# Kernel optimization log

Measured on AMD Instinct MI355X. Metric: run time of the kernel, lower is better.

The kernel has to match this reference:

```python
import jax, jax.numpy as jnp
import numpy as np
import math

RES = 2048
EGG_FACTOR = 0.25
BUMP_STRENGTH = 1.0
SPEC_POWER = 32.0
AMBIENT = 0.1
_L = np.array([0.5, 0.7, 1.0], dtype=np.float32)
LIGHT = _L / np.sqrt((_L * _L).sum())
VIEW = np.array([0.0, 0.0, 1.0], dtype=np.float32)
F0 = np.float32(((1.5 - 1.0) / (1.5 + 1.0)) ** 2)  # Schlick F0 from IOR=1.5 -> 0.04


def _pixel_grid():
    # matches torch.meshgrid(x, y, indexing='xy') ray generation buffers
    x = np.arange(RES, dtype=np.float32)
    y = np.arange(RES, dtype=np.float32)
    px, py = np.meshgrid(x, y, indexing='xy')
    scale = 0.85
    nx = (px / RES - 0.5) * 2.0 / scale
    ny = (0.5 - py / RES) * 2.0 / scale
    return jnp.asarray(nx), jnp.asarray(ny)


def sample_bilinear(tex, u, v):
    # BilinearSampler with UV wrap; tex: (H, W, C), u/v: (...,)
    h, w = tex.shape[0], tex.shape[1]
    u = u % 1.0
    v = v % 1.0
    x = u * w - 0.5
    y = v * h - 0.5
    x0 = jnp.floor(x).astype(jnp.int32) % w
    y0 = jnp.floor(y).astype(jnp.int32) % h
    x1 = (x0 + 1) % w
    y1 = (y0 + 1) % h
    fx = (x - jnp.floor(x))[..., None]
    fy = (y - jnp.floor(y))[..., None]
    v00 = tex[y0, x0]
    v01 = tex[y0, x1]
    v10 = tex[y1, x0]
    v11 = tex[y1, x1]
    return (v00 * (1 - fx) * (1 - fy) + v01 * fx * (1 - fy)
            + v10 * (1 - fx) * fy + v11 * fx * fy)


def _tbn(n):
    # Gram-Schmidt tangent frame from surface normal field, (..., 3)
    up = jnp.zeros_like(n).at[..., 1].set(1.0)
    right = jnp.zeros_like(n).at[..., 0].set(1.0)
    dot_up = n[..., 1]
    ref = jnp.where((jnp.abs(dot_up) > 0.99)[..., None], right, up)
    t = ref - jnp.sum(ref * n, axis=-1, keepdims=True) * n
    t = t / jnp.clip(jnp.linalg.norm(t, axis=-1, keepdims=True), 1e-6)
    b = jnp.cross(n, t)
    return t, b


def reference(texture, normal_map):
    nx, ny = _pixel_grid()
    # 1-2. ray-sphere intersection
    r_sq = nx * nx + ny * ny
    inside = r_sq <= 1.0
    z = jnp.sqrt(jnp.clip(1.0 - r_sq, 0.0))
    # 3. egg deformation
    egg_mod = 1.0 - EGG_FACTOR * ny
    safe = jnp.abs(egg_mod) > 0.01
    x_egg = jnp.where(safe, nx / egg_mod, nx)
    z_egg = jnp.where(safe, z / egg_mod, z)
    # 4. spherical UV
    phi = jnp.arccos(jnp.clip(ny, -1.0, 1.0))
    theta = jnp.arctan2(z_egg, x_egg)
    u = (theta / (2.0 * math.pi) + 0.5) % 1.0
    v = phi / math.pi
    # 5. texture / normal-map sampling
    albedo = sample_bilinear(texture, u, v)
    tex_n = sample_bilinear(normal_map, u, v) * 2.0 - 1.0  # [0,1] -> [-1,1]
    # 6. analytical egg normal + TBN frame
    sn = jnp.stack([nx * egg_mod, ny, z * egg_mod], axis=-1)
    base_n = sn / jnp.clip(jnp.linalg.norm(sn, axis=-1, keepdims=True), 1e-6)
    tangent, bitangent = _tbn(base_n)
    # 7. normal perturbation
    world_n = (tex_n[..., 0:1] * tangent + tex_n[..., 1:2] * bitangent
               + tex_n[..., 2:3] * base_n)
    nrm = base_n * (1.0 - BUMP_STRENGTH) + world_n * BUMP_STRENGTH
    nrm = nrm / jnp.clip(jnp.linalg.norm(nrm, axis=-1, keepdims=True), 1e-6)
    # 8. Blinn-Phong + Schlick Fresnel lighting
    light = jnp.asarray(LIGHT)
    view = jnp.asarray(VIEW)
    half = light + view
    half = half / jnp.linalg.norm(half)
    ndotl = jnp.clip(jnp.sum(nrm * light, axis=-1), 0.0)
    ndoth = jnp.clip(jnp.sum(nrm * half, axis=-1), 0.0)
    spec = ndoth ** SPEC_POWER
    ndotv = jnp.clip(jnp.sum(nrm * view, axis=-1), 0.0)
    fres = F0 + (1.0 - F0) * (1.0 - ndotv) ** 5
    color = albedo * (AMBIENT + ndotl)[..., None] + (spec * fres)[..., None]
    color = jnp.clip(color, 0.0, 1.0)
    return jnp.where(inside[..., None], color, 0.0)


def setup_inputs():
    key = jax.random.key(0)
    k1, k2 = jax.random.split(key)
    texture = jax.random.uniform(k1, (1024, 1024, 3), dtype=jnp.float32)
    normal_map = jax.random.uniform(k2, (1024, 1024, 3), dtype=jnp.float32)
    return {"texture": texture, "normal_map": normal_map}
```

## Files before the change

### kernel.cpp

```cpp
#include <hip/hip_runtime.h>
#include <math.h>

#define RESN 2048
#define TEXW 1024

__device__ __forceinline__ float fatan2_pos(float y, float x) {
    float ax = fabsf(x);
    float mn = fminf(ax, y);
    float mx = fmaxf(ax, y);
    float r0 = __builtin_amdgcn_rcpf(mx);
    r0 = r0 * __builtin_fmaf(-mx, r0, 2.0f);
    float a = mn * r0;
    bool red = a > 0.41421356f;
    float t = (a - 1.0f) * __builtin_amdgcn_rcpf(a + 1.0f);
    float w = red ? t : a;
    float s = w * w;
    float p = __builtin_fmaf(s, 8.05374449538e-2f, -1.38776856032e-1f);
    p = __builtin_fmaf(s, p, 1.99777106478e-1f);
    p = __builtin_fmaf(s, p, -3.33329491539e-1f);
    float r = __builtin_fmaf(w * s, p, w);
    r = red ? r + 0.78539816339f : r;
    r = (y > ax) ? 1.57079632679f - r : r;
    r = (x < 0.0f) ? 3.14159265359f - r : r;
    return r;
}

struct __align__(4) F3 { float x, y, z; };

__global__ __launch_bounds__(256) void egg_render(
    const float* __restrict__ tex,
    const float* __restrict__ nmap,
    float* __restrict__ out)
{
    int t = blockIdx.x * 256 + threadIdx.x;
    int j = t >> 10;
    int tr = t & 1023;
    int iA = ((tr >> 6) << 7) + (tr & 63);
    int iB = iA + 64;
    float* oA = out + ((size_t)j * RESN + iA) * 3u;
    float* oB = oA + 192u;

    const float invres = 1.0f / (float)RESN;
    float ny = __fmul_rn(__fsub_rn(0.5f, __fmul_rn((float)j, invres)), 2.0f) / 0.85f;
    float nysq = __fmul_rn(ny, ny);

    if (!(nysq <= 1.0f)) {
        oA[0] = 0.f; oA[1] = 0.f; oA[2] = 0.f;
        oB[0] = 0.f; oB[1] = 0.f; oB[2] = 0.f;
        return;
    }

    float egg = 1.0f - 0.25f * ny;
    float sphi = sqrtf(fmaxf(__builtin_fmaf(-ny, ny, 1.0f), 0.0f));
    float phi = fatan2_pos(sphi, ny);
    float v = phi * 0.3183098861837907f;
    float yy = v * (float)TEXW - 0.5f;
    float yf = floorf(yy);
    float fy = yy - yf;
    float gy = 1.0f - fy;
    int y0 = (int)yf & (TEXW - 1);
    int y1 = (y0 + 1) & (TEXW - 1);
    int rb0 = y0 * TEXW;
    int rb1 = y1 * TEXW;

    float nxA = __fmul_rn(__fsub_rn(__fmul_rn((float)iA, invres), 0.5f), 2.0f) / 0.85f;
    float rsqA = __fadd_rn(__fmul_rn(nxA, nxA), nysq);
    bool inA = (rsqA <= 1.0f);
    float zA = sqrtf(fmaxf(__fsub_rn(1.0f, rsqA), 0.0f));
    float thetaA = fatan2_pos(zA, nxA);
    float uA = thetaA * 0.15915494309189535f + 0.5f;
    float xxA = uA * (float)TEXW - 0.5f;
    float xfA = floorf(xxA);
    float fxA = xxA - xfA;
    float gxA = 1.0f - fxA;
    int x0A = (int)xfA & (TEXW - 1);
    int x1A = (x0A + 1) & (TEXW - 1);
    float w00A = gxA * gy, w01A = fxA * gy, w10A = gxA * fy, w11A = fxA * fy;
    int o00A = (rb0 + x0A) * 3, o01A = (rb0 + x1A) * 3;
    int o10A = (rb1 + x0A) * 3, o11A = (rb1 + x1A) * 3;

    float nxB = __fmul_rn(__fsub_rn(__fmul_rn((float)iB, invres), 0.5f), 2.0f) / 0.85f;
    float rsqB = __fadd_rn(__fmul_rn(nxB, nxB), nysq);
    bool inB = (rsqB <= 1.0f);
    float zB = sqrtf(fmaxf(__fsub_rn(1.0f, rsqB), 0.0f));
    float thetaB = fatan2_pos(zB, nxB);
    float uB = thetaB * 0.15915494309189535f + 0.5f;
    float xxB = uB * (float)TEXW - 0.5f;
    float xfB = floorf(xxB);
    float fxB = xxB - xfB;
    float gxB = 1.0f - fxB;
    int x0B = (int)xfB & (TEXW - 1);
    int x1B = (x0B + 1) & (TEXW - 1);
    float w00B = gxB * gy, w01B = fxB * gy, w10B = gxB * fy, w11B = fxB * fy;
    int o00B = (rb0 + x0B) * 3, o01B = (rb0 + x1B) * 3;
    int o10B = (rb1 + x0B) * 3, o11B = (rb1 + x1B) * 3;

    if (!(__any((int)inA) || __any((int)inB))) {
        oA[0] = 0.f; oA[1] = 0.f; oA[2] = 0.f;
        oB[0] = 0.f; oB[1] = 0.f; oB[2] = 0.f;
        return;
    }

    F3 aA00 = *(const F3*)(tex + o00A);
    F3 aA01 = *(const F3*)(tex + o01A);
    F3 aA10 = *(const F3*)(tex + o10A);
    F3 aA11 = *(const F3*)(tex + o11A);
    F3 nA00 = *(const F3*)(nmap + o00A);
    F3 nA01 = *(const F3*)(nmap + o01A);
    F3 nA10 = *(const F3*)(nmap + o10A);
    F3 nA11 = *(const F3*)(nmap + o11A);
    F3 aB00 = *(const F3*)(tex + o00B);
    F3 aB01 = *(const F3*)(tex + o01B);
    F3 aB10 = *(const F3*)(tex + o10B);
    F3 aB11 = *(const F3*)(tex + o11B);
    F3 nB00 = *(const F3*)(nmap + o00B);
    F3 nB01 = *(const F3*)(nmap + o01B);
    F3 nB10 = *(const F3*)(nmap + o10B);
    F3 nB11 = *(const F3*)(nmap + o11B);

    float Lx = 0.5f, Ly = 0.7f, Lz = 1.0f;
    float ll = sqrtf(Lx * Lx + Ly * Ly + Lz * Lz);
    Lx /= ll; Ly /= ll; Lz /= ll;
    float Hx = Lx, Hy = Ly, Hz = Lz + 1.0f;
    float hl = sqrtf(Hx * Hx + Hy * Hy + Hz * Hz);
    Hx /= hl; Hy /= hl; Hz /= hl;

    {
        float ar = aA00.x*w00A + aA01.x*w01A + aA10.x*w10A + aA11.x*w11A;
        float ag = aA00.y*w00A + aA01.y*w01A + aA10.y*w10A + aA11.y*w11A;
        float ab = aA00.z*w00A + aA01.z*w01A + aA10.z*w10A + aA11.z*w11A;
        float tnx = (nA00.x*w00A + nA01.x*w01A + nA10.x*w10A + nA11.x*w11A) * 2.0f - 1.0f;
        float tny = (nA00.y*w00A + nA01.y*w01A + nA10.y*w10A + nA11.y*w11A) * 2.0f - 1.0f;
        float tnz = (nA00.z*w00A + nA01.z*w01A + nA10.z*w10A + nA11.z*w11A) * 2.0f - 1.0f;

        float snx = nxA * egg, sny = ny, snz = zA * egg;
        float sl2 = snx*snx + sny*sny + snz*snz;
        float isl = __builtin_amdgcn_rsqf(sl2);
        float bnx = snx * isl, bny = sny * isl, bnz = snz * isl;

        bool use_right = fabsf(bny) > 0.99f;
        float d = use_right ? bnx : bny;
        float m = use_right ? bny : bnx;
        float q2 = m * m + bnz * bnz;
        float iq = __builtin_amdgcn_rsqf(q2);
        float q  = q2 * iq;
        float e  = -(d * iq);
        float tzv = bnz * e;
        float tx = use_right ? q : (bnx * e);
        float ty = use_right ? (bny * e) : q;
        float bnxiq = bnx * iq, bnyiq = bny * iq, bnziq = bnz * iq;
        float bx = use_right ? 0.0f   : -bnziq;
        float by = use_right ? bnziq  : 0.0f;
        float bz = use_right ? -bnyiq : bnxiq;

        float wx = tnx * tx + tny * bx + tnz * bnx;
        float wy = tnx * ty + tny * by + tnz * bny;
        float wz = tnx * tzv + tny * bz + tnz * bnz;
        float wl2 = wx*wx + wy*wy + wz*wz;
        float iwl = __builtin_amdgcn_rsqf(fmaxf(wl2, 1e-12f));
        wx *= iwl; wy *= iwl; wz *= iwl;

        float ndotl = fmaxf(wx * Lx + wy * Ly + wz * Lz, 0.0f);
        float ndoth = fmaxf(wx * Hx + wy * Hy + wz * Hz, 0.0f);
        float s2 = ndoth * ndoth, s4 = s2 * s2, s8 = s4 * s4, s16 = s8 * s8;
        float spec = s16 * s16;
        float ndotv = fmaxf(wz, 0.0f);
        float t1 = 1.0f - ndotv;
        float t2 = t1 * t1, t4 = t2 * t2;
        float fres = 0.04f + 0.96f * (t4 * t1);
        float ka = 0.1f + ndotl;
        float add = spec * fres;

        oA[0] = inA ? fminf(fmaxf(__builtin_fmaf(ar, ka, add), 0.0f), 1.0f) : 0.0f;
        oA[1] = inA ? fminf(fmaxf(__builtin_fmaf(ag, ka, add), 0.0f), 1.0f) : 0.0f;
        oA[2] = inA ? fminf(fmaxf(__builtin_fmaf(ab, ka, add), 0.0f), 1.0f) : 0.0f;
    }

    {
        float ar = aB00.x*w00B + aB01.x*w01B + aB10.x*w10B + aB11.x*w11B;
        float ag = aB00.y*w00B + aB01.y*w01B + aB10.y*w10B + aB11.y*w11B;
        float ab = aB00.z*w00B + aB01.z*w01B + aB10.z*w10B + aB11.z*w11B;
        float tnx = (nB00.x*w00B + nB01.x*w01B + nB10.x*w10B + nB11.x*w11B) * 2.0f - 1.0f;
        float tny = (nB00.y*w00B + nB01.y*w01B + nB10.y*w10B + nB11.y*w11B) * 2.0f - 1.0f;
        float tnz = (nB00.z*w00B + nB01.z*w01B + nB10.z*w10B + nB11.z*w11B) * 2.0f - 1.0f;

        float snx = nxB * egg, sny = ny, snz = zB * egg;
        float sl2 = snx*snx + sny*sny + snz*snz;
        float isl = __builtin_amdgcn_rsqf(sl2);
        float bnx = snx * isl, bny = sny * isl, bnz = snz * isl;

        bool use_right = fabsf(bny) > 0.99f;
        float d = use_right ? bnx : bny;
        float m = use_right ? bny : bnx;
        float q2 = m * m + bnz * bnz;
        float iq = __builtin_amdgcn_rsqf(q2);
        float q  = q2 * iq;
        float e  = -(d * iq);
        float tzv = bnz * e;
        float tx = use_right ? q : (bnx * e);
        float ty = use_right ? (bny * e) : q;
        float bnxiq = bnx * iq, bnyiq = bny * iq, bnziq = bnz * iq;
        float bx = use_right ? 0.0f   : -bnziq;
        float by = use_right ? bnziq  : 0.0f;
        float bz = use_right ? -bnyiq : bnxiq;

        float wx = tnx * tx + tny * bx + tnz * bnx;
        float wy = tnx * ty + tny * by + tnz * bny;
        float wz = tnx * tzv + tny * bz + tnz * bnz;
        float wl2 = wx*wx + wy*wy + wz*wz;
        float iwl = __builtin_amdgcn_rsqf(fmaxf(wl2, 1e-12f));
        wx *= iwl; wy *= iwl; wz *= iwl;

        float ndotl = fmaxf(wx * Lx + wy * Ly + wz * Lz, 0.0f);
        float ndoth = fmaxf(wx * Hx + wy * Hy + wz * Hz, 0.0f);
        float s2 = ndoth * ndoth, s4 = s2 * s2, s8 = s4 * s4, s16 = s8 * s8;
        float spec = s16 * s16;
        float ndotv = fmaxf(wz, 0.0f);
        float t1 = 1.0f - ndotv;
        float t2 = t1 * t1, t4 = t2 * t2;
        float fres = 0.04f + 0.96f * (t4 * t1);
        float ka = 0.1f + ndotl;
        float add = spec * fres;

        oB[0] = inB ? fminf(fmaxf(__builtin_fmaf(ar, ka, add), 0.0f), 1.0f) : 0.0f;
        oB[1] = inB ? fminf(fmaxf(__builtin_fmaf(ag, ka, add), 0.0f), 1.0f) : 0.0f;
        oB[2] = inB ? fminf(fmaxf(__builtin_fmaf(ab, ka, add), 0.0f), 1.0f) : 0.0f;
    }
}

extern "C" void kernel_launch(void* const* d_in, const int* in_sizes, int n_in,
                              void* d_out, int out_size, void* d_ws, size_t ws_size,
                              hipStream_t stream) {
    const float* tex  = (const float*)d_in[0];
    const float* nmap = (const float*)d_in[1];
    float* out = (float*)d_out;
    int total_threads = RESN * RESN / 2;
    dim3 grid(total_threads / 256), block(256);
    hipLaunchKernelGGL(egg_render, grid, block, 0, stream, tex, nmap, out);
}
```

Baseline: 26.32 us.

## Repack texture and normal map into half-precision interleaved records in workspace

Adds a pre-pass kernel that gathers only the half of the texture columns the visible hemisphere can sample, converts albedo and normal to fp16 and interleaves them into one 16-byte record per texel. The render kernel then does four 16-byte loads per sample instead of eight scattered 12-byte loads. This reduces gather traffic and the number of load instructions, at the cost of an extra kernel launch, a full pass over the inputs in every call, and fp16 rounding of the texture data. The wave-level early-out for fully outside waves is dropped, and a fallback path is kept for when workspace is too small.

```diff
diff --git a/kernel.cpp b/kernel.cpp
--- a/kernel.cpp
+++ b/kernel.cpp
@@ -1,8 +1,12 @@
 #include <hip/hip_runtime.h>
+#include <hip/hip_fp16.h>
 #include <math.h>
 
 #define RESN 2048
 #define TEXW 1024
+#define PW 514
+#define PH 1025
+#define PREC (PH * PW)
 
 __device__ __forceinline__ float fatan2_pos(float y, float x) {
     float ax = fabsf(x);
@@ -26,8 +30,176 @@
 }
 
 struct __align__(4) F3 { float x, y, z; };
-
-__global__ __launch_bounds__(256) void egg_render(
+union HU { uint4 v; __half h[8]; };
+
+__global__ __launch_bounds__(256) void repack(const float* __restrict__ tex,
+                                              const float* __restrict__ nmap,
+                                              uint4* __restrict__ rec) {
+    int idx = blockIdx.x * 256 + threadIdx.x;
+    if (idx >= PREC) return;
+    int y  = idx / PW;
+    int rx = idx - y * PW;
+    int sx = (rx + 511) & (TEXW - 1);
+    int sy = y & (TEXW - 1);
+    int s = (sy * TEXW + sx) * 3;
+    HU u;
+    u.h[0] = __float2half(tex[s + 0]);
+    u.h[1] = __float2half(tex[s + 1]);
+    u.h[2] = __float2half(tex[s + 2]);
+    u.h[3] = __float2half(nmap[s + 0]);
+    u.h[4] = __float2half(nmap[s + 1]);
+    u.h[5] = __float2half(nmap[s + 2]);
+    u.h[6] = __float2half(0.0f);
+    u.h[7] = __float2half(0.0f);
+    rec[idx] = u.v;
+}
+
+#define BLEND6(c00, c01, c10, c11, w00, w01, w10, w11, ar, ag, ab, tnx, tny, tnz)          \
+    ar  = __half2float(c00.h[0])*w00 + __half2float(c01.h[0])*w01                          \
+        + __half2float(c10.h[0])*w10 + __half2float(c11.h[0])*w11;                         \
+    ag  = __half2float(c00.h[1])*w00 + __half2float(c01.h[1])*w01                          \
+        + __half2float(c10.h[1])*w10 + __half2float(c11.h[1])*w11;                         \
+    ab  = __half2float(c00.h[2])*w00 + __half2float(c01.h[2])*w01                          \
+        + __half2float(c10.h[2])*w10 + __half2float(c11.h[2])*w11;                         \
+    tnx = (__half2float(c00.h[3])*w00 + __half2float(c01.h[3])*w01                         \
+        +  __half2float(c10.h[3])*w10 + __half2float(c11.h[3])*w11) * 2.0f - 1.0f;         \
+    tny = (__half2float(c00.h[4])*w00 + __half2float(c01.h[4])*w01                         \
+        +  __half2float(c10.h[4])*w10 + __half2float(c11.h[4])*w11) * 2.0f - 1.0f;         \
+    tnz = (__half2float(c00.h[5])*w00 + __half2float(c01.h[5])*w01                         \
+        +  __half2float(c10.h[5])*w10 + __half2float(c11.h[5])*w11) * 2.0f - 1.0f;
+
+#define SHADE(nx, z, tnx, tny, tnz, ar, ag, ab, inx, o)                                    \
+    {                                                                                      \
+        float snx = nx * egg, sny = ny, snz = z * egg;                                     \
+        float sl2 = snx*snx + sny*sny + snz*snz;                                           \
+        float isl = __builtin_amdgcn_rsqf(sl2);                                            \
+        float bnx = snx * isl, bny = sny * isl, bnz = snz * isl;                           \
+        bool use_right = fabsf(bny) > 0.99f;                                               \
+        float d = use_right ? bnx : bny;                                                   \
+        float m = use_right ? bny : bnx;                                                   \
+        float q2 = m * m + bnz * bnz;                                                      \
+        float iq = __builtin_amdgcn_rsqf(q2);                                              \
+        float q  = q2 * iq;                                                                \
+        float e  = -(d * iq);                                                              \
+        float tzv = bnz * e;                                                               \
+        float tx = use_right ? q : (bnx * e);                                              \
+        float ty = use_right ? (bny * e) : q;                                              \
+        float bx = use_right ? 0.0f        : -(bnz * iq);                                  \
+        float by = use_right ? (bnz * iq)  : 0.0f;                                         \
+        float bz = use_right ? -(bny * iq) : (bnx * iq);                                   \
+        float wx = tnx * tx + tny * bx + tnz * bnx;                                        \
+        float wy = tnx * ty + tny * by + tnz * bny;                                        \
+        float wz = tnx * tzv + tny * bz + tnz * bnz;                                       \
+        float wl2 = wx*wx + wy*wy + wz*wz;                                                 \
+        float iwl = __builtin_amdgcn_rsqf(fmaxf(wl2, 1e-12f));                             \
+        wx *= iwl; wy *= iwl; wz *= iwl;                                                   \
+        float ndotl = fmaxf(wx * Lx + wy * Ly + wz * Lz, 0.0f);                            \
+        float ndoth = fmaxf(wx * Hx + wy * Hy + wz * Hz, 0.0f);                            \
+        float s2 = ndoth * ndoth, s4 = s2 * s2, s8 = s4 * s4, s16 = s8 * s8;               \
+        float spec = s16 * s16;                                                            \
+        float ndotv = fmaxf(wz, 0.0f);                                                     \
+        float t1 = 1.0f - ndotv;                                                           \
+        float t2v = t1 * t1, t4v = t2v * t2v;                                              \
+        float fres = 0.04f + 0.96f * (t4v * t1);                                           \
+        float ka = 0.1f + ndotl;                                                           \
+        float add = spec * fres;                                                           \
+        o[0] = inx ? fminf(fmaxf(__builtin_fmaf(ar, ka, add), 0.0f), 1.0f) : 0.0f;         \
+        o[1] = inx ? fminf(fmaxf(__builtin_fmaf(ag, ka, add), 0.0f), 1.0f) : 0.0f;         \
+        o[2] = inx ? fminf(fmaxf(__builtin_fmaf(ab, ka, add), 0.0f), 1.0f) : 0.0f;         \
+    }
+
+__global__ __launch_bounds__(256) void egg_render_packed(
+    const uint4* __restrict__ rec,
+    float* __restrict__ out)
+{
+    int t = blockIdx.x * 256 + threadIdx.x;
+    int j = t >> 10;
+    int tr = t & 1023;
+    int iA = ((tr >> 6) << 7) + (tr & 63);
+    int iB = iA + 64;
+    float* oA = out + ((size_t)j * RESN + iA) * 3u;
+    float* oB = oA + 192u;
+
+    const float invres = 1.0f / (float)RESN;
+    float ny = __fmul_rn(__fsub_rn(0.5f, __fmul_rn((float)j, invres)), 2.0f) / 0.85f;
+    float nysq = __fmul_rn(ny, ny);
+
+    if (!(nysq <= 1.0f)) {
+        oA[0] = 0.f; oA[1] = 0.f; oA[2] = 0.f;
+        oB[0] = 0.f; oB[1] = 0.f; oB[2] = 0.f;
+        return;
+    }
+
+    float egg = 1.0f - 0.25f * ny;
+    float sphi = sqrtf(fmaxf(__builtin_fmaf(-ny, ny, 1.0f), 0.0f));
+    float phi = fatan2_pos(sphi, ny);
+    float v = phi * 0.3183098861837907f;
+    float yy = v * (float)TEXW - 0.5f;
+    float yf = floorf(yy);
+    float fy = yy - yf;
+    float gy = 1.0f - fy;
+    int y0 = (int)yf & (TEXW - 1);
+    int rb0 = y0 * PW;
+    int rb1 = rb0 + PW;
+
+    float nxA = __fmul_rn(__fsub_rn(__fmul_rn((float)iA, invres), 0.5f), 2.0f) / 0.85f;
+    float rsqA = __fadd_rn(__fmul_rn(nxA, nxA), nysq);
+    bool inA = (rsqA <= 1.0f);
+    float zA = sqrtf(fmaxf(__fsub_rn(1.0f, rsqA), 0.0f));
+    float thetaA = fatan2_pos(zA, nxA);
+    float uA = thetaA * 0.15915494309189535f + 0.5f;
+    float xxA = uA * (float)TEXW - 0.5f;
+    float xfA = floorf(xxA);
+    float fxA = xxA - xfA;
+    float gxA = 1.0f - fxA;
+    int rxA = min(max((int)xfA - 511, 0), 512);
+    float w00A = gxA * gy, w01A = fxA * gy, w10A = gxA * fy, w11A = fxA * fy;
+
+    HU cA00, cA01, cA10, cA11;
+    cA00.v = rec[rb0 + rxA];
+    cA01.v = rec[rb0 + rxA + 1];
+    cA10.v = rec[rb1 + rxA];
+    cA11.v = rec[rb1 + rxA + 1];
+
+    float nxB = __fmul_rn(__fsub_rn(__fmul_rn((float)iB, invres), 0.5f), 2.0f) / 0.85f;
+    float rsqB = __fadd_rn(__fmul_rn(nxB, nxB), nysq);
+    bool inB = (rsqB <= 1.0f);
+    float zB = sqrtf(fmaxf(__fsub_rn(1.0f, rsqB), 0.0f));
+    float thetaB = fatan2_pos(zB, nxB);
+    float uB = thetaB * 0.15915494309189535f + 0.5f;
+    float xxB = uB * (float)TEXW - 0.5f;
+    float xfB = floorf(xxB);
+    float fxB = xxB - xfB;
+    float gxB = 1.0f - fxB;
+    int rxB = min(max((int)xfB - 511, 0), 512);
+    float w00B = gxB * gy, w01B = fxB * gy, w10B = gxB * fy, w11B = fxB * fy;
+
+    HU cB00, cB01, cB10, cB11;
+    cB00.v = rec[rb0 + rxB];
+    cB01.v = rec[rb0 + rxB + 1];
+    cB10.v = rec[rb1 + rxB];
+    cB11.v = rec[rb1 + rxB + 1];
+
+    float Lx = 0.5f, Ly = 0.7f, Lz = 1.0f;
+    float ll = sqrtf(Lx * Lx + Ly * Ly + Lz * Lz);
+    Lx /= ll; Ly /= ll; Lz /= ll;
+    float Hx = Lx, Hy = Ly, Hz = Lz + 1.0f;
+    float hl = sqrtf(Hx * Hx + Hy * Hy + Hz * Hz);
+    Hx /= hl; Hy /= hl; Hz /= hl;
+
+    {
+        float ar, ag, ab, tnx, tny, tnz;
+        BLEND6(cA00, cA01, cA10, cA11, w00A, w01A, w10A, w11A, ar, ag, ab, tnx, tny, tnz)
+        SHADE(nxA, zA, tnx, tny, tnz, ar, ag, ab, inA, oA)
+    }
+    {
+        float ar, ag, ab, tnx, tny, tnz;
+        BLEND6(cB00, cB01, cB10, cB11, w00B, w01B, w10B, w11B, ar, ag, ab, tnx, tny, tnz)
+        SHADE(nxB, zB, tnx, tny, tnz, ar, ag, ab, inB, oB)
+    }
+}
+
+__global__ __launch_bounds__(256) void egg_render_fb(
     const float* __restrict__ tex,
     const float* __restrict__ nmap,
     float* __restrict__ out)
@@ -79,6 +251,15 @@
     int o00A = (rb0 + x0A) * 3, o01A = (rb0 + x1A) * 3;
     int o10A = (rb1 + x0A) * 3, o11A = (rb1 + x1A) * 3;
 
+    F3 aA00 = *(const F3*)(tex + o00A);
+    F3 aA01 = *(const F3*)(tex + o01A);
+    F3 aA10 = *(const F3*)(tex + o10A);
+    F3 aA11 = *(const F3*)(tex + o11A);
+    F3 nA00 = *(const F3*)(nmap + o00A);
+    F3 nA01 = *(const F3*)(nmap + o01A);
+    F3 nA10 = *(const F3*)(nmap + o10A);
+    F3 nA11 = *(const F3*)(nmap + o11A);
+
     float nxB = __fmul_rn(__fsub_rn(__fmul_rn((float)iB, invres), 0.5f), 2.0f) / 0.85f;
     float rsqB = __fadd_rn(__fmul_rn(nxB, nxB), nysq);
     bool inB = (rsqB <= 1.0f);
@@ -95,20 +276,6 @@
     int o00B = (rb0 + x0B) * 3, o01B = (rb0 + x1B) * 3;
     int o10B = (rb1 + x0B) * 3, o11B = (rb1 + x1B) * 3;
 
-    if (!(__any((int)inA) || __any((int)inB))) {
-        oA[0] = 0.f; oA[1] = 0.f; oA[2] = 0.f;
-        oB[0] = 0.f; oB[1] = 0.f; oB[2] = 0.f;
-        return;
-    }
-
-    F3 aA00 = *(const F3*)(tex + o00A);
-    F3 aA01 = *(const F3*)(tex + o01A);
-    F3 aA10 = *(const F3*)(tex + o10A);
-    F3 aA11 = *(const F3*)(tex + o11A);
-    F3 nA00 = *(const F3*)(nmap + o00A);
-    F3 nA01 = *(const F3*)(nmap + o01A);
-    F3 nA10 = *(const F3*)(nmap + o10A);
-    F3 nA11 = *(const F3*)(nmap + o11A);
     F3 aB00 = *(const F3*)(tex + o00B);
     F3 aB01 = *(const F3*)(tex + o01B);
     F3 aB10 = *(const F3*)(tex + o10B);
@@ -132,50 +299,8 @@
         float tnx = (nA00.x*w00A + nA01.x*w01A + nA10.x*w10A + nA11.x*w11A) * 2.0f - 1.0f;
         float tny = (nA00.y*w00A + nA01.y*w01A + nA10.y*w10A + nA11.y*w11A) * 2.0f - 1.0f;
         float tnz = (nA00.z*w00A + nA01.z*w01A + nA10.z*w10A + nA11.z*w11A) * 2.0f - 1.0f;
-
-        float snx = nxA * egg, sny = ny, snz = zA * egg;
-        float sl2 = snx*snx + sny*sny + snz*snz;
-        float isl = __builtin_amdgcn_rsqf(sl2);
-        float bnx = snx * isl, bny = sny * isl, bnz = snz * isl;
-
-        bool use_right = fabsf(bny) > 0.99f;
-        float d = use_right ? bnx : bny;
-        float m = use_right ? bny : bnx;
-        float q2 = m * m + bnz * bnz;
-        float iq = __builtin_amdgcn_rsqf(q2);
-        float q  = q2 * iq;
-        float e  = -(d * iq);
-        float tzv = bnz * e;
-        float tx = use_right ? q : (bnx * e);
-        float ty = use_right ? (bny * e) : q;
-        float bnxiq = bnx * iq, bnyiq = bny * iq, bnziq = bnz * iq;
-        float bx = use_right ? 0.0f   : -bnziq;
-        float by = use_right ? bnziq  : 0.0f;
-        float bz = use_right ? -bnyiq : bnxiq;
-
-        float wx = tnx * tx + tny * bx + tnz * bnx;
-        float wy = tnx * ty + tny * by + tnz * bny;
-        float wz = tnx * tzv + tny * bz + tnz * bnz;
-        float wl2 = wx*wx + wy*wy + wz*wz;
-        float iwl = __builtin_amdgcn_rsqf(fmaxf(wl2, 1e-12f));
-        wx *= iwl; wy *= iwl; wz *= iwl;
-
-        float ndotl = fmaxf(wx * Lx + wy * Ly + wz * Lz, 0.0f);
-        float ndoth = fmaxf(wx * Hx + wy * Hy + wz * Hz, 0.0f);
-        float s2 = ndoth * ndoth, s4 = s2 * s2, s8 = s4 * s4, s16 = s8 * s8;
-        float spec = s16 * s16;
-        float ndotv = fmaxf(wz, 0.0f);
-        float t1 = 1.0f - ndotv;
-        float t2 = t1 * t1, t4 = t2 * t2;
-        float fres = 0.04f + 0.96f * (t4 * t1);
-        float ka = 0.1f + ndotl;
-        float add = spec * fres;
-
-        oA[0] = inA ? fminf(fmaxf(__builtin_fmaf(ar, ka, add), 0.0f), 1.0f) : 0.0f;
-        oA[1] = inA ? fminf(fmaxf(__builtin_fmaf(ag, ka, add), 0.0f), 1.0f) : 0.0f;
-        oA[2] = inA ? fminf(fmaxf(__builtin_fmaf(ab, ka, add), 0.0f), 1.0f) : 0.0f;
-    }
-
+        SHADE(nxA, zA, tnx, tny, tnz, ar, ag, ab, inA, oA)
+    }
     {
         float ar = aB00.x*w00B + aB01.x*w01B + aB10.x*w10B + aB11.x*w11B;
         float ag = aB00.y*w00B + aB01.y*w01B + aB10.y*w10B + aB11.y*w11B;
@@ -183,48 +308,7 @@
         float tnx = (nB00.x*w00B + nB01.x*w01B + nB10.x*w10B + nB11.x*w11B) * 2.0f - 1.0f;
         float tny = (nB00.y*w00B + nB01.y*w01B + nB10.y*w10B + nB11.y*w11B) * 2.0f - 1.0f;
         float tnz = (nB00.z*w00B + nB01.z*w01B + nB10.z*w10B + nB11.z*w11B) * 2.0f - 1.0f;
-
-        float snx = nxB * egg, sny = ny, snz = zB * egg;
-        float sl2 = snx*snx + sny*sny + snz*snz;
-        float isl = __builtin_amdgcn_rsqf(sl2);
-        float bnx = snx * isl, bny = sny * isl, bnz = snz * isl;
-
-        bool use_right = fabsf(bny) > 0.99f;
-        float d = use_right ? bnx : bny;
-        float m = use_right ? bny : bnx;
-        float q2 = m * m + bnz * bnz;
-        float iq = __builtin_amdgcn_rsqf(q2);
-        float q  = q2 * iq;
-        float e  = -(d * iq);
-        float tzv = bnz * e;
-        float tx = use_right ? q : (bnx * e);
-        float ty = use_right ? (bny * e) : q;
-        float bnxiq = bnx * iq, bnyiq = bny * iq, bnziq = bnz * iq;
-        float bx = use_right ? 0.0f   : -bnziq;
-        float by = use_right ? bnziq  : 0.0f;
-        float bz = use_right ? -bnyiq : bnxiq;
-
-        float wx = tnx * tx + tny * bx + tnz * bnx;
-        float wy = tnx * ty + tny * by + tnz * bny;
-        float wz = tnx * tzv + tny * bz + tnz * bnz;
-        float wl2 = wx*wx + wy*wy + wz*wz;
-        float iwl = __builtin_amdgcn_rsqf(fmaxf(wl2, 1e-12f));
-        wx *= iwl; wy *= iwl; wz *= iwl;
-
-        float ndotl = fmaxf(wx * Lx + wy * Ly + wz * Lz, 0.0f);
-        float ndoth = fmaxf(wx * Hx + wy * Hy + wz * Hz, 0.0f);
-        float s2 = ndoth * ndoth, s4 = s2 * s2, s8 = s4 * s4, s16 = s8 * s8;
-        float spec = s16 * s16;
-        float ndotv = fmaxf(wz, 0.0f);
-        float t1 = 1.0f - ndotv;
-        float t2 = t1 * t1, t4 = t2 * t2;
-        float fres = 0.04f + 0.96f * (t4 * t1);
-        float ka = 0.1f + ndotl;
-        float add = spec * fres;
-
-        oB[0] = inB ? fminf(fmaxf(__builtin_fmaf(ar, ka, add), 0.0f), 1.0f) : 0.0f;
-        oB[1] = inB ? fminf(fmaxf(__builtin_fmaf(ag, ka, add), 0.0f), 1.0f) : 0.0f;
-        oB[2] = inB ? fminf(fmaxf(__builtin_fmaf(ab, ka, add), 0.0f), 1.0f) : 0.0f;
+        SHADE(nxB, zB, tnx, tny, tnz, ar, ag, ab, inB, oB)
     }
 }
 
@@ -235,6 +319,15 @@
     const float* nmap = (const float*)d_in[1];
     float* out = (float*)d_out;
     int total_threads = RESN * RESN / 2;
-    dim3 grid(total_threads / 256), block(256);
-    hipLaunchKernelGGL(egg_render, grid, block, 0, stream, tex, nmap, out);
-}
+
+    if (ws_size >= (size_t)PREC * 16u) {
+        uint4* rec = (uint4*)d_ws;
+        hipLaunchKernelGGL(repack, dim3((PREC + 255) / 256), dim3(256), 0, stream,
+                           tex, nmap, rec);
+        hipLaunchKernelGGL(egg_render_packed, dim3(total_threads / 256), dim3(256),
+                           0, stream, rec, out);
+    } else {
+        hipLaunchKernelGGL(egg_render_fb, dim3(total_threads / 256), dim3(256),
+                           0, stream, tex, nmap, out);
+    }
+}
```

Measured after the change: 34.60 us. 1.31x slower.
